# Performance work log

Measured on AMD Instinct MI355X. Metric: run time of the kernel, lower is better.

## Reference

```python
import jax, jax.numpy as jnp
import numpy as np

WS = 3  # window size


def _shift_stack(t_pad, D, H, W):
    # t_pad: [B, nh, hd, D+2p, H+2p, W+2p] -> [B, nh, hd, D, H, W, WS**3]
    slabs = [t_pad[..., i:i + D, j:j + H, l:l + W]
             for i in range(WS) for j in range(WS) for l in range(WS)]
    return jnp.stack(slabs, axis=-1)


def setup_inputs() -> dict:
    key = jax.random.key(0)
    ks = jax.random.split(key, 6)
    B, C, D, H, W = 2, 128, 24, 24, 24
    nh, hd = 4, 32
    return {
        "x": jax.random.normal(ks[0], (B, C, D, H, W), dtype=jnp.float32),
        "qkv_w": jax.random.normal(ks[1], (3 * C, C), dtype=jnp.float32) * 0.02,
        "qkv_b": jax.random.normal(ks[2], (3 * C,), dtype=jnp.float32) * 0.02,
        "proj_w": jax.random.normal(ks[3], (C, C), dtype=jnp.float32) * 0.02,
        "proj_b": jax.random.normal(ks[4], (C,), dtype=jnp.float32) * 0.02,
        "pos_embed": jax.random.normal(ks[5], (hd, WS, WS, WS), dtype=jnp.float32) * 0.02,
    }


def reference(x, qkv_w, qkv_b, proj_w, proj_b, pos_embed):
    B, C, D, H, W = x.shape
    hd = pos_embed.shape[0]
    nh = C // hd
    scale = hd ** -0.5
    pad = WS // 2

    # 1x1x1 Conv3d == pointwise linear over channel dim
    qkv = jnp.einsum('bcdhw,oc->bodhw', x, qkv_w) + qkv_b[None, :, None, None, None]
    q, k, v = jnp.split(qkv, 3, axis=1)
    q = q.reshape(B, nh, hd, D, H, W)
    k = k.reshape(B, nh, hd, D, H, W)
    v = v.reshape(B, nh, hd, D, H, W)

    pcfg = [(0, 0)] * 3 + [(pad, pad)] * 3
    k_pad = jnp.pad(k, pcfg)
    v_pad = jnp.pad(v, pcfg)

    # windows: [B, nh, hd, D, H, W, WS^3]; window center of q == q itself
    k_win = _shift_stack(k_pad, D, H, W)
    v_win = _shift_stack(v_pad, D, H, W)
    k_win = k_win + pos_embed.reshape(hd, WS ** 3)[None, None, :, None, None, None, :]

    scores = jnp.einsum('bncdhw,bncdhwk->bndhwk', q, k_win) * scale
    attn = jax.nn.softmax(scores, axis=-1)
    out = jnp.einsum('bndhwk,bncdhwk->bncdhw', attn, v_win)
    out = out.reshape(B, C, D, H, W)
    return jnp.einsum('bcdhw,oc->bodhw', out, proj_w) + proj_b[None, :, None, None, None]
```

## Files before the change

### kernel.cpp

```cpp
#include <hip/hip_runtime.h>
#include <hip/hip_bf16.h>
#include <hip/hip_fp16.h>

#define SVOX 13824
#define CIN 128
#define NHEAD 4
#define HDIM 32

#define BD 2
#define BH 4
#define BW 8
#define WD (BD+2)
#define WH (BH+2)
#define WW (BW+2)
#define NWIN (WD*WH*WW)

typedef __attribute__((ext_vector_type(8))) short short8;
typedef __attribute__((ext_vector_type(4))) float f32x4;
#if defined(__has_builtin)
#if __has_builtin(__builtin_amdgcn_fdot2_f32_bf16)
#define HAVE_DOT2BF 1
typedef __attribute__((ext_vector_type(2))) __bf16 bf16x2;
#endif
#if __has_builtin(__builtin_amdgcn_mov_dpp)
#define HAVE_DPP 1
#endif
#if __has_builtin(__builtin_amdgcn_cvt_pkrtz)
#define HAVE_PKRTZ 1
#endif
#endif

__device__ __forceinline__ unsigned short f2bf(float x) {
    unsigned u = __float_as_uint(x);
    u += 0x7FFFu + ((u >> 16) & 1u);
    return (unsigned short)(u >> 16);
}
__device__ __forceinline__ float dot2bf(unsigned a, unsigned b, float c) {
#ifdef HAVE_DOT2BF
    return __builtin_amdgcn_fdot2_f32_bf16(__builtin_bit_cast(bf16x2, a),
                                           __builtin_bit_cast(bf16x2, b), c, false);
#else
    return __uint_as_float(a << 16) * __uint_as_float(b << 16)
         + __uint_as_float(a & 0xffff0000u) * __uint_as_float(b & 0xffff0000u) + c;
#endif
}
template<int CTRL>
__device__ __forceinline__ float quad_dpp(float x) {
#ifdef HAVE_DPP
    return __int_as_float(__builtin_amdgcn_mov_dpp(__float_as_int(x), CTRL, 0xf, 0xf, true));
#else
    return __shfl_xor(x, (CTRL == 0xB1) ? 1 : 2);
#endif
}
__device__ __forceinline__ __half2 u2h2(unsigned u) {
    union { unsigned u; __half2 h; } c; c.u = u; return c.h;
}
__device__ __forceinline__ __half2 splat_h2(float x) {
#ifdef HAVE_PKRTZ
    auto v = __builtin_amdgcn_cvt_pkrtz(x, x);
    union { decltype(v) a; __half2 h; } c; c.a = v; return c.h;
#else
    return __float2half2_rn(x);
#endif
}
__device__ __forceinline__ unsigned short f2h(float x) {
    return __builtin_bit_cast(unsigned short, (_Float16)x);
}

__global__ __launch_bounds__(256) void qkv_gemm(
    const float* __restrict__ X,
    const float* __restrict__ W,
    const float* __restrict__ bias,
    const float* __restrict__ pos,
    unsigned* __restrict__ pe_out,
    ushort* __restrict__ q_out,
    ushort* __restrict__ k_out,
    ushort* __restrict__ v_out)
{
    __shared__ __align__(16) unsigned char smem[26624];
    ushort* Wb = (ushort*)smem;
    ushort* Xs = (ushort*)(smem + 17408);
    float*  T  = (float*)smem;

    const int t    = threadIdx.x;
    const int s0   = blockIdx.x * 64;
    const int o0   = blockIdx.y * 64;
    const int b    = blockIdx.z;
    const int lane = t & 63;
    const int wid  = t >> 6;
    const int l15  = lane & 15;
    const int g4   = lane >> 4;
    const int wm   = (wid >> 1) * 32;
    const int wn   = (wid & 1) * 32;

    if (blockIdx.x == 0 && blockIdx.y == 0 && blockIdx.z == 0 && t < 27 * 16) {
        int w = t >> 4, cp = t & 15;
        unsigned lo = f2bf(pos[(2 * cp) * 27 + w]);
        unsigned hi = f2bf(pos[(2 * cp + 1) * 27 + w]);
        pe_out[t] = lo | (hi << 16);
    }

    #pragma unroll
    for (int i = 0; i < 8; i++) {
        int f = t + i * 256;
        int row = f >> 5, c4 = f & 31;
        float4 w = *(const float4*)(W + (size_t)(o0 + row) * CIN + c4 * 4);
        ushort4 u;
        u.x = f2bf(w.x); u.y = f2bf(w.y); u.z = f2bf(w.z); u.w = f2bf(w.w);
        *(ushort4*)(Wb + row * 136 + c4 * 4) = u;
    }

    f32x4 acc[2][2];
    #pragma unroll
    for (int mf = 0; mf < 2; mf++)
        #pragma unroll
        for (int nf = 0; nf < 2; nf++)
            acc[mf][nf] = (f32x4){0.f, 0.f, 0.f, 0.f};

    const int sx = t & 63;
    const int kg = t >> 6;

    for (int chunk = 0; chunk < 2; chunk++) {
        __syncthreads();
        ushort xk[16];
        #pragma unroll
        for (int i = 0; i < 16; i++) {
            int k = kg * 16 + i;
            xk[i] = f2bf(X[((size_t)b * CIN + chunk * 64 + k) * SVOX + s0 + sx]);
        }
        #pragma unroll
        for (int j = 0; j < 2; j++) {
            short8 v;
            #pragma unroll
            for (int e = 0; e < 8; e++) v[e] = (short)xk[j * 8 + e];
            *(short8*)(Xs + sx * 72 + kg * 16 + j * 8) = v;
        }
        __syncthreads();

        #pragma unroll
        for (int ks = 0; ks < 2; ks++) {
            short8 Af[2], Bf[2];
            #pragma unroll
            for (int mf = 0; mf < 2; mf++)
                Af[mf] = *(const short8*)(Wb + (wm + mf * 16 + l15) * 136 + chunk * 64 + ks * 32 + g4 * 8);
            #pragma unroll
            for (int nf = 0; nf < 2; nf++)
                Bf[nf] = *(const short8*)(Xs + (wn + nf * 16 + l15) * 72 + ks * 32 + g4 * 8);
            #pragma unroll
            for (int mf = 0; mf < 2; mf++)
                #pragma unroll
                for (int nf = 0; nf < 2; nf++)
                    acc[mf][nf] = __builtin_amdgcn_mfma_f32_16x16x32_bf16(Af[mf], Bf[nf], acc[mf][nf], 0, 0, 0);
        }
    }

    __syncthreads();
    #pragma unroll
    for (int mf = 0; mf < 2; mf++)
        #pragma unroll
        for (int nf = 0; nf < 2; nf++) {
            int s  = wn + nf * 16 + l15;
            int mb = wm + mf * 16 + g4 * 4;
            *(f32x4*)(T + s * 68 + mb) = acc[mf][nf];
        }
    __syncthreads();
    #pragma unroll
    for (int i = 0; i < 4; i++) {
        int f = t + i * 256;
        int og = f & 15, sl = f >> 4;
        float4 v = *(float4*)(T + sl * 68 + og * 4);
        int o_g = o0 + og * 4;
        v.x += bias[o_g]; v.y += bias[o_g + 1]; v.z += bias[o_g + 2]; v.w += bias[o_g + 3];
        int part = o_g >> 7, pc = o_g & 127;
        int head = pc >> 5, ic = pc & 31;
        size_t base = (((size_t)b * NHEAD + head) * SVOX + s0 + sl) * HDIM + ic;
        ushort4 u;
        if (part == 2) {
            u.x = f2h(v.x); u.y = f2h(v.y); u.z = f2h(v.z); u.w = f2h(v.w);
        } else {
            u.x = f2bf(v.x); u.y = f2bf(v.y); u.z = f2bf(v.z); u.w = f2bf(v.w);
        }
        ushort* dst = (part == 0) ? q_out : (part == 1) ? k_out : v_out;
        *(ushort4*)(dst + base) = u;
    }
}

__global__ __launch_bounds__(256, 5) void attn_kernel(
    const ushort* __restrict__ qbf,
    const ushort* __restrict__ kbf,
    const ushort* __restrict__ vhf,
    const unsigned* __restrict__ pe_g,
    ushort* __restrict__ aout)
{
    __shared__ __align__(16) ushort Kl[NWIN * 32];
    __shared__ __align__(16) ushort Vl[NWIN * 32];

    const int t = threadIdx.x;
    const int br = blockIdx.x;
    const int n  = blockIdx.y;
    const int b  = blockIdx.z;
    const int bw_ = br % 3;
    const int bh_ = (br / 3) % 6;
    const int bd_ = br / 18;
    const int d0 = bd_ * BD, h0 = bh_ * BH, w0 = bw_ * BW;

    const ushort* kb = kbf + ((size_t)b * NHEAD + n) * (size_t)SVOX * HDIM;
    const ushort* vb = vhf + ((size_t)b * NHEAD + n) * (size_t)SVOX * HDIM;

    #pragma unroll
    for (int i = 0; i < 4; i++) {
        int f = t + i * 256;
        if (f < NWIN * 4) {
            int u = f >> 2, ch = f & 3;
            int ud = u / (WH * WW);
            int r  = u - ud * (WH * WW);
            int uh = r / WW;
            int uw = r - uh * WW;
            int gd = d0 + ud - 1, gh = h0 + uh - 1, gw = w0 + uw - 1;
            bool valid = ((unsigned)gd < 24u) & ((unsigned)gh < 24u) & ((unsigned)gw < 24u);
            size_t gsv = valid ? (size_t)(gd * 576 + gh * 24 + gw) : 0;
            uint4 kv = *(const uint4*)(kb + gsv * HDIM + ch * 8);
            uint4 vv = *(const uint4*)(vb + gsv * HDIM + ch * 8);
            if (!valid) { kv = make_uint4(0,0,0,0); vv = make_uint4(0,0,0,0); }
            *(uint4*)(Kl + u * 32 + ch * 8) = kv;
            *(uint4*)(Vl + u * 32 + ch * 8) = vv;
        }
    }

    const int p   = t >> 2;
    const int sub = t & 3;
    const int pw = p & 7, ph = (p >> 3) & 3, pd = p >> 5;
    const int sv = (d0 + pd) * 576 + (h0 + ph) * 24 + w0 + pw;
    uint4 qpk = *(const uint4*)(qbf + (((size_t)b * NHEAD + n) * SVOX + sv) * HDIM + sub * 8);

    float sc[27];
    #pragma unroll
    for (int s = 0; s < 27; s++) {
        uint4 pp = *(const uint4*)(pe_g + s * 16 + sub * 4);
        float a = dot2bf(qpk.x, pp.x, 0.f);
        a = dot2bf(qpk.y, pp.y, a);
        a = dot2bf(qpk.z, pp.z, a);
        a = dot2bf(qpk.w, pp.w, a);
        sc[s] = a;
    }

    __syncthreads();

    const int wc = (pd + 1) * (WH * WW) + (ph + 1) * WW + (pw + 1);
    const ushort* Kbase = Kl + wc * 32 + sub * 8;

    #pragma unroll
    for (int s = 0; s < 27; s++) {
        const int di = s / 9 - 1, dj = (s / 3) % 3 - 1, dl = s % 3 - 1;
        const int off = (di * (WH * WW) + dj * WW + dl) * 32;
        uint4 kk = *(const uint4*)(Kbase + off);
        float a = sc[s];
        a = dot2bf(qpk.x, kk.x, a);
        a = dot2bf(qpk.y, kk.y, a);
        a = dot2bf(qpk.z, kk.z, a);
        a = dot2bf(qpk.w, kk.w, a);
        sc[s] = a;
    }

    #pragma unroll
    for (int s = 0; s < 27; s++) {
        sc[s] += quad_dpp<0xB1>(sc[s]);
        sc[s] += quad_dpp<0x4E>(sc[s]);
    }

    float m3[9];
    #pragma unroll
    for (int j = 0; j < 9; j++)
        m3[j] = fmaxf(fmaxf(sc[3*j], sc[3*j+1]), sc[3*j+2]);
    float m9a = fmaxf(fmaxf(m3[0], m3[1]), m3[2]);
    float m9b = fmaxf(fmaxf(m3[3], m3[4]), m3[5]);
    float m9c = fmaxf(fmaxf(m3[6], m3[7]), m3[8]);
    float mx  = fmaxf(fmaxf(m9a, m9b), m9c);

    const float KS = 0.17677669529663687f * 1.4426950408889634f;
    float sum = 0.f;
    #pragma unroll
    for (int s = 0; s < 27; s++) {
        float e = exp2f((sc[s] - mx) * KS);
        sc[s] = e;
        sum += e;
    }
    float inv = 1.f / sum;

    const ushort* Vbase = Vl + wc * 32 + sub * 8;
    __half2 o2[4];
    __half2 hz = __float2half2_rn(0.f);
    o2[0] = hz; o2[1] = hz; o2[2] = hz; o2[3] = hz;
    #pragma unroll
    for (int s = 0; s < 27; s++) {
        const int di = s / 9 - 1, dj = (s / 3) % 3 - 1, dl = s % 3 - 1;
        const int off = (di * (WH * WW) + dj * WW + dl) * 32;
        uint4 vv = *(const uint4*)(Vbase + off);
        __half2 p2 = splat_h2(sc[s]);
        o2[0] = __hfma2(p2, u2h2(vv.x), o2[0]);
        o2[1] = __hfma2(p2, u2h2(vv.y), o2[1]);
        o2[2] = __hfma2(p2, u2h2(vv.z), o2[2]);
        o2[3] = __hfma2(p2, u2h2(vv.w), o2[3]);
    }

    float o[8];
    #pragma unroll
    for (int j = 0; j < 4; j++) {
        o[2*j]   = __low2float(o2[j]);
        o[2*j+1] = __high2float(o2[j]);
    }

    uint4 ou;
    ou.x = (unsigned)f2bf(o[0] * inv) | ((unsigned)f2bf(o[1] * inv) << 16);
    ou.y = (unsigned)f2bf(o[2] * inv) | ((unsigned)f2bf(o[3] * inv) << 16);
    ou.z = (unsigned)f2bf(o[4] * inv) | ((unsigned)f2bf(o[5] * inv) << 16);
    ou.w = (unsigned)f2bf(o[6] * inv) | ((unsigned)f2bf(o[7] * inv) << 16);
    *(uint4*)(aout + ((size_t)b * SVOX + sv) * CIN + n * HDIM + sub * 8) = ou;
}

__global__ __launch_bounds__(256) void proj_gemm(
    const ushort* __restrict__ Xa,
    const float* __restrict__ W,
    const float* __restrict__ bias,
    float* __restrict__ out)
{
    __shared__ __align__(16) unsigned char smem[34816];
    ushort* Wb = (ushort*)smem;
    ushort* Xs = (ushort*)(smem + 17408);
    float*  T  = (float*)smem;

    const int t    = threadIdx.x;
    const int s0   = blockIdx.x * 64;
    const int o0   = blockIdx.y * 64;
    const int b    = blockIdx.z;
    const int lane = t & 63;
    const int wid  = t >> 6;
    const int l15  = lane & 15;
    const int g4   = lane >> 4;
    const int wm   = (wid >> 1) * 32;
    const int wn   = (wid & 1) * 32;

    #pragma unroll
    for (int i = 0; i < 8; i++) {
        int f = t + i * 256;
        int row = f >> 5, c4 = f & 31;
        float4 w = *(const float4*)(W + (size_t)(o0 + row) * CIN + c4 * 4);
        ushort4 u;
        u.x = f2bf(w.x); u.y = f2bf(w.y); u.z = f2bf(w.z); u.w = f2bf(w.w);
        *(ushort4*)(Wb + row * 136 + c4 * 4) = u;
    }
    #pragma unroll
    for (int i = 0; i < 4; i++) {
        int f = t + i * 256;
        int row = f >> 4, c8 = f & 15;
        *(uint4*)(Xs + row * 136 + c8 * 8) =
            *(const uint4*)(Xa + ((size_t)b * SVOX + s0 + row) * CIN + c8 * 8);
    }
    __syncthreads();

    f32x4 acc[2][2];
    #pragma unroll
    for (int mf = 0; mf < 2; mf++)
        #pragma unroll
        for (int nf = 0; nf < 2; nf++)
            acc[mf][nf] = (f32x4){0.f, 0.f, 0.f, 0.f};

    #pragma unroll
    for (int ks = 0; ks < 4; ks++) {
        short8 Af[2], Bf[2];
        #pragma unroll
        for (int mf = 0; mf < 2; mf++)
            Af[mf] = *(const short8*)(Wb + (wm + mf * 16 + l15) * 136 + ks * 32 + g4 * 8);
        #pragma unroll
        for (int nf = 0; nf < 2; nf++)
            Bf[nf] = *(const short8*)(Xs + (wn + nf * 16 + l15) * 136 + ks * 32 + g4 * 8);
        #pragma unroll
        for (int mf = 0; mf < 2; mf++)
            #pragma unroll
            for (int nf = 0; nf < 2; nf++)
                acc[mf][nf] = __builtin_amdgcn_mfma_f32_16x16x32_bf16(Af[mf], Bf[nf], acc[mf][nf], 0, 0, 0);
    }

    __syncthreads();
    #pragma unroll
    for (int mf = 0; mf < 2; mf++)
        #pragma unroll
        for (int nf = 0; nf < 2; nf++) {
            int s  = wn + nf * 16 + l15;
            int mb = wm + mf * 16 + g4 * 4;
            #pragma unroll
            for (int r = 0; r < 4; r++)
                T[(mb + r) * 72 + s] = acc[mf][nf][r];
        }
    __syncthreads();
    #pragma unroll
    for (int i = 0; i < 4; i++) {
        int f = t + i * 256;
        int s4 = f & 15, m = f >> 4;
        float4 v = *(float4*)(T + m * 72 + s4 * 4);
        float bi = bias[o0 + m];
        v.x += bi; v.y += bi; v.z += bi; v.w += bi;
        *(float4*)(out + ((size_t)b * CIN + o0 + m) * SVOX + s0 + s4 * 4) = v;
    }
}

extern "C" void kernel_launch(void* const* d_in, const int* in_sizes, int n_in,
                              void* d_out, int out_size, void* d_ws, size_t ws_size,
                              hipStream_t stream) {
    const float* x      = (const float*)d_in[0];
    const float* qkv_w  = (const float*)d_in[1];
    const float* qkv_b  = (const float*)d_in[2];
    const float* proj_w = (const float*)d_in[3];
    const float* proj_b = (const float*)d_in[4];
    const float* pos    = (const float*)d_in[5];
    float* out = (float*)d_out;

    const size_t HSZ = (size_t)2 * NHEAD * SVOX * HDIM;
    ushort* qb  = (ushort*)d_ws;
    ushort* kbp = qb + HSZ;
    ushort* vbp = kbp + HSZ;
    ushort* attn_o = vbp + HSZ;
    unsigned* pe_p = (unsigned*)(attn_o + HSZ);

    qkv_gemm<<<dim3(SVOX/64, 384/64, 2), 256, 0, stream>>>(x, qkv_w, qkv_b, pos, pe_p, qb, kbp, vbp);
    attn_kernel<<<dim3(216, NHEAD, 2), 256, 0, stream>>>(qb, kbp, vbp, pe_p, attn_o);
    proj_gemm<<<dim3(SVOX/64, CIN/64, 2), 256, 0, stream>>>(attn_o, proj_w, proj_b, out);
}
```

Before: 46.32 us.

## Read V directly from global memory, drop LDS V tile and softmax max

Removes the shared-memory V staging and instead gathers the 27 neighbour V vectors straight from global memory, using a per-voxel validity mask so out-of-bounds neighbours get zero weight. This halves LDS use, so the launch-bounds occupancy hint is raised from 5 to 6 blocks. It also drops the max subtraction in softmax, which saves ALU work but risks exp overflow if scores get large, though that is unlikely at these input scales. Global V reads now depend on L2/L1 hits in place of LDS reuse.

```diff
diff --git a/kernel.cpp b/kernel.cpp
--- a/kernel.cpp
+++ b/kernel.cpp
@@ -185,7 +185,7 @@
     }
 }
 
-__global__ __launch_bounds__(256, 5) void attn_kernel(
+__global__ __launch_bounds__(256, 6) void attn_kernel(
     const ushort* __restrict__ qbf,
     const ushort* __restrict__ kbf,
     const ushort* __restrict__ vhf,
@@ -193,7 +193,6 @@
     ushort* __restrict__ aout)
 {
     __shared__ __align__(16) ushort Kl[NWIN * 32];
-    __shared__ __align__(16) ushort Vl[NWIN * 32];
 
     const int t = threadIdx.x;
     const int br = blockIdx.x;
@@ -220,18 +219,38 @@
             bool valid = ((unsigned)gd < 24u) & ((unsigned)gh < 24u) & ((unsigned)gw < 24u);
             size_t gsv = valid ? (size_t)(gd * 576 + gh * 24 + gw) : 0;
             uint4 kv = *(const uint4*)(kb + gsv * HDIM + ch * 8);
-            uint4 vv = *(const uint4*)(vb + gsv * HDIM + ch * 8);
-            if (!valid) { kv = make_uint4(0,0,0,0); vv = make_uint4(0,0,0,0); }
+            if (!valid) kv = make_uint4(0, 0, 0, 0);
             *(uint4*)(Kl + u * 32 + ch * 8) = kv;
-            *(uint4*)(Vl + u * 32 + ch * 8) = vv;
         }
     }
 
     const int p   = t >> 2;
     const int sub = t & 3;
     const int pw = p & 7, ph = (p >> 3) & 3, pd = p >> 5;
-    const int sv = (d0 + pd) * 576 + (h0 + ph) * 24 + w0 + pw;
+    const int dd0 = d0 + pd, hh0 = h0 + ph, ww0 = w0 + pw;
+    const int sv = dd0 * 576 + hh0 * 24 + ww0;
     uint4 qpk = *(const uint4*)(qbf + (((size_t)b * NHEAD + n) * SVOX + sv) * HDIM + sub * 8);
+
+    const int doff[27] = {
+        -601,-600,-599,-577,-576,-575,-553,-552,-551,
+         -25, -24, -23,  -1,   0,   1,  23,  24,  25,
+         551, 552, 553, 575, 576, 577, 599, 600, 601
+    };
+
+    unsigned vm = 0;
+    {
+        int widx = 0;
+        #pragma unroll
+        for (int di = -1; di <= 1; di++)
+        #pragma unroll
+        for (int dj = -1; dj <= 1; dj++)
+        #pragma unroll
+        for (int dl = -1; dl <= 1; dl++) {
+            if (((unsigned)(dd0 + di) < 24u) & ((unsigned)(hh0 + dj) < 24u) & ((unsigned)(ww0 + dl) < 24u))
+                vm |= 1u << widx;
+            widx++;
+        }
+    }
 
     float sc[27];
     #pragma unroll
@@ -268,35 +287,27 @@
         sc[s] += quad_dpp<0x4E>(sc[s]);
     }
 
-    float m3[9];
-    #pragma unroll
-    for (int j = 0; j < 9; j++)
-        m3[j] = fmaxf(fmaxf(sc[3*j], sc[3*j+1]), sc[3*j+2]);
-    float m9a = fmaxf(fmaxf(m3[0], m3[1]), m3[2]);
-    float m9b = fmaxf(fmaxf(m3[3], m3[4]), m3[5]);
-    float m9c = fmaxf(fmaxf(m3[6], m3[7]), m3[8]);
-    float mx  = fmaxf(fmaxf(m9a, m9b), m9c);
-
     const float KS = 0.17677669529663687f * 1.4426950408889634f;
     float sum = 0.f;
     #pragma unroll
     for (int s = 0; s < 27; s++) {
-        float e = exp2f((sc[s] - mx) * KS);
+        float e = exp2f(sc[s] * KS);
         sc[s] = e;
         sum += e;
     }
     float inv = 1.f / sum;
 
-    const ushort* Vbase = Vl + wc * 32 + sub * 8;
+    const ushort* Vbase = vb + (size_t)sv * HDIM + sub * 8;
     __half2 o2[4];
     __half2 hz = __float2half2_rn(0.f);
     o2[0] = hz; o2[1] = hz; o2[2] = hz; o2[3] = hz;
     #pragma unroll
     for (int s = 0; s < 27; s++) {
-        const int di = s / 9 - 1, dj = (s / 3) % 3 - 1, dl = s % 3 - 1;
-        const int off = (di * (WH * WW) + dj * WW + dl) * 32;
+        bool valid = (vm >> s) & 1u;
+        int off = valid ? doff[s] * 32 : 0;
         uint4 vv = *(const uint4*)(Vbase + off);
-        __half2 p2 = splat_h2(sc[s]);
+        float pr = valid ? sc[s] : 0.f;
+        __half2 p2 = splat_h2(pr);
         o2[0] = __hfma2(p2, u2h2(vv.x), o2[0]);
         o2[1] = __hfma2(p2, u2h2(vv.y), o2[1]);
         o2[2] = __hfma2(p2, u2h2(vv.z), o2[2]);
```

Measured after the change: 105.3 us. 127% more time.

## Split attention scores across quad lanes by window offset instead of channels

Applied to the files above, without the earlier changes.

Each of the four lanes per voxel now computes full 32-channel dot products for about 7 of the 27 window offsets, rather than a quarter of the channels for all 27. This removes the per-score cross-lane DPP reductions and cuts the per-thread score register footprint. Normalized probabilities are then shared to the quad with ds_bpermute during the V accumulation. The softmax max-subtraction is dropped, which relies on scores being small enough not to overflow exp. The attention output is now written as fp16 and the projection GEMM switches to f16 MFMA to match.

```diff
diff --git a/kernel.cpp b/kernel.cpp
--- a/kernel.cpp
+++ b/kernel.cpp
@@ -16,6 +16,7 @@
 #define NWIN (WD*WH*WW)
 
 typedef __attribute__((ext_vector_type(8))) short short8;
+typedef __attribute__((ext_vector_type(8))) _Float16 half8;
 typedef __attribute__((ext_vector_type(4))) float f32x4;
 #if defined(__has_builtin)
 #if __has_builtin(__builtin_amdgcn_fdot2_f32_bf16)
@@ -55,12 +56,13 @@
 __device__ __forceinline__ __half2 u2h2(unsigned u) {
     union { unsigned u; __half2 h; } c; c.u = u; return c.h;
 }
-__device__ __forceinline__ __half2 splat_h2(float x) {
+__device__ __forceinline__ unsigned splat_h2u(float x) {
 #ifdef HAVE_PKRTZ
     auto v = __builtin_amdgcn_cvt_pkrtz(x, x);
-    union { decltype(v) a; __half2 h; } c; c.a = v; return c.h;
+    union { decltype(v) a; unsigned u; } c; c.a = v; return c.u;
 #else
-    return __float2half2_rn(x);
+    __half2 h = __float2half2_rn(x);
+    union { __half2 h; unsigned u; } c; c.h = h; return c.u;
 #endif
 }
 __device__ __forceinline__ unsigned short f2h(float x) {
@@ -194,6 +196,7 @@
 {
     __shared__ __align__(16) ushort Kl[NWIN * 32];
     __shared__ __align__(16) ushort Vl[NWIN * 32];
+    __shared__ int doffT[32];
 
     const int t = threadIdx.x;
     const int br = blockIdx.x;
@@ -203,6 +206,11 @@
     const int bh_ = (br / 3) % 6;
     const int bd_ = br / 18;
     const int d0 = bd_ * BD, h0 = bh_ * BH, w0 = bw_ * BW;
+
+    if (t < 27) {
+        int di = t / 9 - 1, dj = (t / 3) % 3 - 1, dl = t % 3 - 1;
+        doffT[t] = (di * (WH * WW) + dj * WW + dl) * 64;
+    }
 
     const ushort* kb = kbf + ((size_t)b * NHEAD + n) * (size_t)SVOX * HDIM;
     const ushort* vb = vhf + ((size_t)b * NHEAD + n) * (size_t)SVOX * HDIM;
@@ -231,61 +239,68 @@
     const int sub = t & 3;
     const int pw = p & 7, ph = (p >> 3) & 3, pd = p >> 5;
     const int sv = (d0 + pd) * 576 + (h0 + ph) * 24 + w0 + pw;
-    uint4 qpk = *(const uint4*)(qbf + (((size_t)b * NHEAD + n) * SVOX + sv) * HDIM + sub * 8);
-
-    float sc[27];
-    #pragma unroll
-    for (int s = 0; s < 27; s++) {
-        uint4 pp = *(const uint4*)(pe_g + s * 16 + sub * 4);
-        float a = dot2bf(qpk.x, pp.x, 0.f);
-        a = dot2bf(qpk.y, pp.y, a);
-        a = dot2bf(qpk.z, pp.z, a);
-        a = dot2bf(qpk.w, pp.w, a);
-        sc[s] = a;
+
+    const ushort* qrow = qbf + (((size_t)b * NHEAD + n) * SVOX + sv) * HDIM;
+    uint4 q0 = *(const uint4*)(qrow);
+    uint4 q1 = *(const uint4*)(qrow + 8);
+    uint4 q2 = *(const uint4*)(qrow + 16);
+    uint4 q3 = *(const uint4*)(qrow + 24);
+
+    float sc[7];
+    #pragma unroll
+    for (int i = 0; i < 7; i++) {
+        int s = 4 * i + sub; s = (s > 26) ? 26 : s;
+        const uint4* pp = (const uint4*)(pe_g + s * 16);
+        uint4 p0 = pp[0], p1 = pp[1], p2 = pp[2], p3 = pp[3];
+        float a = dot2bf(q0.x, p0.x, 0.f);
+        a = dot2bf(q0.y, p0.y, a); a = dot2bf(q0.z, p0.z, a); a = dot2bf(q0.w, p0.w, a);
+        a = dot2bf(q1.x, p1.x, a); a = dot2bf(q1.y, p1.y, a); a = dot2bf(q1.z, p1.z, a); a = dot2bf(q1.w, p1.w, a);
+        a = dot2bf(q2.x, p2.x, a); a = dot2bf(q2.y, p2.y, a); a = dot2bf(q2.z, p2.z, a); a = dot2bf(q2.w, p2.w, a);
+        a = dot2bf(q3.x, p3.x, a); a = dot2bf(q3.y, p3.y, a); a = dot2bf(q3.z, p3.z, a); a = dot2bf(q3.w, p3.w, a);
+        sc[i] = a;
     }
 
     __syncthreads();
 
     const int wc = (pd + 1) * (WH * WW) + (ph + 1) * WW + (pw + 1);
-    const ushort* Kbase = Kl + wc * 32 + sub * 8;
-
-    #pragma unroll
-    for (int s = 0; s < 27; s++) {
-        const int di = s / 9 - 1, dj = (s / 3) % 3 - 1, dl = s % 3 - 1;
-        const int off = (di * (WH * WW) + dj * WW + dl) * 32;
-        uint4 kk = *(const uint4*)(Kbase + off);
-        float a = sc[s];
-        a = dot2bf(qpk.x, kk.x, a);
-        a = dot2bf(qpk.y, kk.y, a);
-        a = dot2bf(qpk.z, kk.z, a);
-        a = dot2bf(qpk.w, kk.w, a);
-        sc[s] = a;
-    }
-
-    #pragma unroll
-    for (int s = 0; s < 27; s++) {
-        sc[s] += quad_dpp<0xB1>(sc[s]);
-        sc[s] += quad_dpp<0x4E>(sc[s]);
-    }
-
-    float m3[9];
-    #pragma unroll
-    for (int j = 0; j < 9; j++)
-        m3[j] = fmaxf(fmaxf(sc[3*j], sc[3*j+1]), sc[3*j+2]);
-    float m9a = fmaxf(fmaxf(m3[0], m3[1]), m3[2]);
-    float m9b = fmaxf(fmaxf(m3[3], m3[4]), m3[5]);
-    float m9c = fmaxf(fmaxf(m3[6], m3[7]), m3[8]);
-    float mx  = fmaxf(fmaxf(m9a, m9b), m9c);
+    const char* KrowB = (const char*)Kl + wc * 64;
+
+    #pragma unroll
+    for (int i = 0; i < 7; i++) {
+        int s = 4 * i + sub; s = (s > 26) ? 26 : s;
+        const ushort* kp = (const ushort*)(KrowB + doffT[s]);
+        uint4 k0 = *(const uint4*)(kp);
+        uint4 k1 = *(const uint4*)(kp + 8);
+        uint4 k2 = *(const uint4*)(kp + 16);
+        uint4 k3 = *(const uint4*)(kp + 24);
+        float a = sc[i];
+        a = dot2bf(q0.x, k0.x, a); a = dot2bf(q0.y, k0.y, a); a = dot2bf(q0.z, k0.z, a); a = dot2bf(q0.w, k0.w, a);
+        a = dot2bf(q1.x, k1.x, a); a = dot2bf(q1.y, k1.y, a); a = dot2bf(q1.z, k1.z, a); a = dot2bf(q1.w, k1.w, a);
+        a = dot2bf(q2.x, k2.x, a); a = dot2bf(q2.y, k2.y, a); a = dot2bf(q2.z, k2.z, a); a = dot2bf(q2.w, k2.w, a);
+        a = dot2bf(q3.x, k3.x, a); a = dot2bf(q3.y, k3.y, a); a = dot2bf(q3.z, k3.z, a); a = dot2bf(q3.w, k3.w, a);
+        sc[i] = a;
+    }
 
     const float KS = 0.17677669529663687f * 1.4426950408889634f;
-    float sum = 0.f;
-    #pragma unroll
-    for (int s = 0; s < 27; s++) {
-        float e = exp2f((sc[s] - mx) * KS);
-        sc[s] = e;
-        sum += e;
-    }
-    float inv = 1.f / sum;
+    float e[7];
+    float sm = 0.f;
+    #pragma unroll
+    for (int i = 0; i < 7; i++) {
+        float ee = exp2f(sc[i] * KS);
+        if (4 * i + sub > 26) ee = 0.f;
+        e[i] = ee;
+        sm += ee;
+    }
+    sm += quad_dpp<0xB1>(sm);
+    sm += quad_dpp<0x4E>(sm);
+    float inv = 1.f / sm;
+
+    unsigned ph2[7];
+    #pragma unroll
+    for (int i = 0; i < 7; i++)
+        ph2[i] = splat_h2u(e[i] * inv);
+
+    const int lb = ((t & 63) & ~3) * 4;
 
     const ushort* Vbase = Vl + wc * 32 + sub * 8;
     __half2 o2[4];
@@ -295,27 +310,18 @@
     for (int s = 0; s < 27; s++) {
         const int di = s / 9 - 1, dj = (s / 3) % 3 - 1, dl = s % 3 - 1;
         const int off = (di * (WH * WW) + dj * WW + dl) * 32;
+        int src = __builtin_amdgcn_ds_bpermute(lb + (s & 3) * 4, (int)ph2[s >> 2]);
+        __half2 p2 = u2h2((unsigned)src);
         uint4 vv = *(const uint4*)(Vbase + off);
-        __half2 p2 = splat_h2(sc[s]);
         o2[0] = __hfma2(p2, u2h2(vv.x), o2[0]);
         o2[1] = __hfma2(p2, u2h2(vv.y), o2[1]);
         o2[2] = __hfma2(p2, u2h2(vv.z), o2[2]);
         o2[3] = __hfma2(p2, u2h2(vv.w), o2[3]);
     }
 
-    float o[8];
-    #pragma unroll
-    for (int j = 0; j < 4; j++) {
-        o[2*j]   = __low2float(o2[j]);
-        o[2*j+1] = __high2float(o2[j]);
-    }
-
-    uint4 ou;
-    ou.x = (unsigned)f2bf(o[0] * inv) | ((unsigned)f2bf(o[1] * inv) << 16);
-    ou.y = (unsigned)f2bf(o[2] * inv) | ((unsigned)f2bf(o[3] * inv) << 16);
-    ou.z = (unsigned)f2bf(o[4] * inv) | ((unsigned)f2bf(o[5] * inv) << 16);
-    ou.w = (unsigned)f2bf(o[6] * inv) | ((unsigned)f2bf(o[7] * inv) << 16);
-    *(uint4*)(aout + ((size_t)b * SVOX + sv) * CIN + n * HDIM + sub * 8) = ou;
+    union { __half2 h[4]; uint4 u; } ou;
+    ou.h[0] = o2[0]; ou.h[1] = o2[1]; ou.h[2] = o2[2]; ou.h[3] = o2[3];
+    *(uint4*)(aout + ((size_t)b * SVOX + sv) * CIN + n * HDIM + sub * 8) = ou.u;
 }
 
 __global__ __launch_bounds__(256) void proj_gemm(
@@ -346,7 +352,7 @@
         int row = f >> 5, c4 = f & 31;
         float4 w = *(const float4*)(W + (size_t)(o0 + row) * CIN + c4 * 4);
         ushort4 u;
-        u.x = f2bf(w.x); u.y = f2bf(w.y); u.z = f2bf(w.z); u.w = f2bf(w.w);
+        u.x = f2h(w.x); u.y = f2h(w.y); u.z = f2h(w.z); u.w = f2h(w.w);
         *(ushort4*)(Wb + row * 136 + c4 * 4) = u;
     }
     #pragma unroll
@@ -367,18 +373,18 @@
 
     #pragma unroll
     for (int ks = 0; ks < 4; ks++) {
-        short8 Af[2], Bf[2];
+        half8 Af[2], Bf[2];
         #pragma unroll
         for (int mf = 0; mf < 2; mf++)
-            Af[mf] = *(const short8*)(Wb + (wm + mf * 16 + l15) * 136 + ks * 32 + g4 * 8);
+            Af[mf] = __builtin_bit_cast(half8, *(const short8*)(Wb + (wm + mf * 16 + l15) * 136 + ks * 32 + g4 * 8));
         #pragma unroll
         for (int nf = 0; nf < 2; nf++)
-            Bf[nf] = *(const short8*)(Xs + (wn + nf * 16 + l15) * 136 + ks * 32 + g4 * 8);
+            Bf[nf] = __builtin_bit_cast(half8, *(const short8*)(Xs + (wn + nf * 16 + l15) * 136 + ks * 32 + g4 * 8));
         #pragma unroll
         for (int mf = 0; mf < 2; mf++)
             #pragma unroll
             for (int nf = 0; nf < 2; nf++)
-                acc[mf][nf] = __builtin_amdgcn_mfma_f32_16x16x32_bf16(Af[mf], Bf[nf], acc[mf][nf], 0, 0, 0);
+                acc[mf][nf] = __builtin_amdgcn_mfma_f32_16x16x32_f16(Af[mf], Bf[nf], acc[mf][nf], 0, 0, 0);
     }
 
     __syncthreads();
```

Result: slower. 48.45 us (+4.6%).

## Process two adjacent query voxels per thread to share K/V window loads

Applied to the files above, without the earlier changes.

Each thread now handles an even/odd pair of neighbouring voxels along W. The pair shares the overlapping K and V LDS reads, 36 loads instead of 54. The tile doubles in H (BH 8) to keep 256 threads, the halo ratio drops, and the grid halves. Softmax drops the max subtraction and the output is written as fp16, with proj_gemm switched to fp16 MFMA to match. Risks are overflow in exp without max subtraction, higher register pressure (launch bounds 5 to 3) and fp16 precision changes.

```diff
diff --git a/kernel.cpp b/kernel.cpp
--- a/kernel.cpp
+++ b/kernel.cpp
@@ -8,7 +8,7 @@
 #define HDIM 32
 
 #define BD 2
-#define BH 4
+#define BH 8
 #define BW 8
 #define WD (BD+2)
 #define WH (BH+2)
@@ -16,6 +16,7 @@
 #define NWIN (WD*WH*WW)
 
 typedef __attribute__((ext_vector_type(8))) short short8;
+typedef __attribute__((ext_vector_type(8))) _Float16 half8;
 typedef __attribute__((ext_vector_type(4))) float f32x4;
 #if defined(__has_builtin)
 #if __has_builtin(__builtin_amdgcn_fdot2_f32_bf16)
@@ -43,6 +44,11 @@
     return __uint_as_float(a << 16) * __uint_as_float(b << 16)
          + __uint_as_float(a & 0xffff0000u) * __uint_as_float(b & 0xffff0000u) + c;
 #endif
+}
+__device__ __forceinline__ float dot4(uint4 a, uint4 b, float c) {
+    c = dot2bf(a.x, b.x, c); c = dot2bf(a.y, b.y, c);
+    c = dot2bf(a.z, b.z, c); c = dot2bf(a.w, b.w, c);
+    return c;
 }
 template<int CTRL>
 __device__ __forceinline__ float quad_dpp(float x) {
@@ -185,7 +191,7 @@
     }
 }
 
-__global__ __launch_bounds__(256, 5) void attn_kernel(
+__global__ __launch_bounds__(256, 3) void attn_kernel(
     const ushort* __restrict__ qbf,
     const ushort* __restrict__ kbf,
     const ushort* __restrict__ vhf,
@@ -200,15 +206,15 @@
     const int n  = blockIdx.y;
     const int b  = blockIdx.z;
     const int bw_ = br % 3;
-    const int bh_ = (br / 3) % 6;
-    const int bd_ = br / 18;
+    const int bh_ = (br / 3) % 3;
+    const int bd_ = br / 9;
     const int d0 = bd_ * BD, h0 = bh_ * BH, w0 = bw_ * BW;
 
     const ushort* kb = kbf + ((size_t)b * NHEAD + n) * (size_t)SVOX * HDIM;
     const ushort* vb = vhf + ((size_t)b * NHEAD + n) * (size_t)SVOX * HDIM;
 
     #pragma unroll
-    for (int i = 0; i < 4; i++) {
+    for (int i = 0; i < 7; i++) {
         int f = t + i * 256;
         if (f < NWIN * 4) {
             int u = f >> 2, ch = f & 3;
@@ -227,95 +233,101 @@
         }
     }
 
-    const int p   = t >> 2;
+    const int qd  = t >> 2;
     const int sub = t & 3;
-    const int pw = p & 7, ph = (p >> 3) & 3, pd = p >> 5;
-    const int sv = (d0 + pd) * 576 + (h0 + ph) * 24 + w0 + pw;
-    uint4 qpk = *(const uint4*)(qbf + (((size_t)b * NHEAD + n) * SVOX + sv) * HDIM + sub * 8);
-
-    float sc[27];
+    const int pw2 = qd & 3;
+    const int ph  = (qd >> 2) & 7;
+    const int pd  = qd >> 5;
+    const int pwE = pw2 * 2;
+    const int svE = (d0 + pd) * 576 + (h0 + ph) * 24 + w0 + pwE;
+
+    const ushort* qrow = qbf + (((size_t)b * NHEAD + n) * SVOX + svE) * HDIM + sub * 8;
+    uint4 qE = *(const uint4*)(qrow);
+    uint4 qO = *(const uint4*)(qrow + HDIM);
+
+    float scE[27], scO[27];
     #pragma unroll
     for (int s = 0; s < 27; s++) {
         uint4 pp = *(const uint4*)(pe_g + s * 16 + sub * 4);
-        float a = dot2bf(qpk.x, pp.x, 0.f);
-        a = dot2bf(qpk.y, pp.y, a);
-        a = dot2bf(qpk.z, pp.z, a);
-        a = dot2bf(qpk.w, pp.w, a);
-        sc[s] = a;
-    }
-
-    __syncthreads();
-
-    const int wc = (pd + 1) * (WH * WW) + (ph + 1) * WW + (pw + 1);
-    const ushort* Kbase = Kl + wc * 32 + sub * 8;
+        scE[s] = dot4(qE, pp, 0.f);
+        scO[s] = dot4(qO, pp, 0.f);
+    }
+
+    __syncthreads();
+
+    const int wcE = (pd + 1) * (WH * WW) + (ph + 1) * WW + (pwE + 1);
+    const ushort* Kbase = Kl + wcE * 32 + sub * 8;
+
+    #pragma unroll
+    for (int di = 0; di < 3; di++)
+    #pragma unroll
+    for (int dj = 0; dj < 3; dj++)
+    #pragma unroll
+    for (int dlp = 0; dlp < 4; dlp++) {
+        const int off = ((di - 1) * (WH * WW) + (dj - 1) * WW + (dlp - 1)) * 32;
+        uint4 kk = *(const uint4*)(Kbase + off);
+        if (dlp <= 2) { const int s = (di * 3 + dj) * 3 + dlp;     scE[s] = dot4(qE, kk, scE[s]); }
+        if (dlp >= 1) { const int s = (di * 3 + dj) * 3 + dlp - 1; scO[s] = dot4(qO, kk, scO[s]); }
+    }
 
     #pragma unroll
     for (int s = 0; s < 27; s++) {
-        const int di = s / 9 - 1, dj = (s / 3) % 3 - 1, dl = s % 3 - 1;
-        const int off = (di * (WH * WW) + dj * WW + dl) * 32;
-        uint4 kk = *(const uint4*)(Kbase + off);
-        float a = sc[s];
-        a = dot2bf(qpk.x, kk.x, a);
-        a = dot2bf(qpk.y, kk.y, a);
-        a = dot2bf(qpk.z, kk.z, a);
-        a = dot2bf(qpk.w, kk.w, a);
-        sc[s] = a;
-    }
-
+        scE[s] += quad_dpp<0xB1>(scE[s]);
+        scE[s] += quad_dpp<0x4E>(scE[s]);
+        scO[s] += quad_dpp<0xB1>(scO[s]);
+        scO[s] += quad_dpp<0x4E>(scO[s]);
+    }
+
+    const float KS = 0.17677669529663687f * 1.4426950408889634f;
+    float sumE = 0.f, sumO = 0.f;
     #pragma unroll
     for (int s = 0; s < 27; s++) {
-        sc[s] += quad_dpp<0xB1>(sc[s]);
-        sc[s] += quad_dpp<0x4E>(sc[s]);
-    }
-
-    float m3[9];
-    #pragma unroll
-    for (int j = 0; j < 9; j++)
-        m3[j] = fmaxf(fmaxf(sc[3*j], sc[3*j+1]), sc[3*j+2]);
-    float m9a = fmaxf(fmaxf(m3[0], m3[1]), m3[2]);
-    float m9b = fmaxf(fmaxf(m3[3], m3[4]), m3[5]);
-    float m9c = fmaxf(fmaxf(m3[6], m3[7]), m3[8]);
-    float mx  = fmaxf(fmaxf(m9a, m9b), m9c);
-
-    const float KS = 0.17677669529663687f * 1.4426950408889634f;
-    float sum = 0.f;
-    #pragma unroll
-    for (int s = 0; s < 27; s++) {
-        float e = exp2f((sc[s] - mx) * KS);
-        sc[s] = e;
-        sum += e;
-    }
-    float inv = 1.f / sum;
-
-    const ushort* Vbase = Vl + wc * 32 + sub * 8;
-    __half2 o2[4];
+        float eE = exp2f(scE[s] * KS);
+        float eO = exp2f(scO[s] * KS);
+        scE[s] = eE; sumE += eE;
+        scO[s] = eO; sumO += eO;
+    }
+    float invE = 1.f / sumE, invO = 1.f / sumO;
+    #pragma unroll
+    for (int s = 0; s < 27; s++) { scE[s] *= invE; scO[s] *= invO; }
+
+    const ushort* Vbase = Vl + wcE * 32 + sub * 8;
+    __half2 oE[4], oO[4];
     __half2 hz = __float2half2_rn(0.f);
-    o2[0] = hz; o2[1] = hz; o2[2] = hz; o2[3] = hz;
-    #pragma unroll
-    for (int s = 0; s < 27; s++) {
-        const int di = s / 9 - 1, dj = (s / 3) % 3 - 1, dl = s % 3 - 1;
-        const int off = (di * (WH * WW) + dj * WW + dl) * 32;
+    oE[0]=hz; oE[1]=hz; oE[2]=hz; oE[3]=hz;
+    oO[0]=hz; oO[1]=hz; oO[2]=hz; oO[3]=hz;
+    #pragma unroll
+    for (int di = 0; di < 3; di++)
+    #pragma unroll
+    for (int dj = 0; dj < 3; dj++)
+    #pragma unroll
+    for (int dlp = 0; dlp < 4; dlp++) {
+        const int off = ((di - 1) * (WH * WW) + (dj - 1) * WW + (dlp - 1)) * 32;
         uint4 vv = *(const uint4*)(Vbase + off);
-        __half2 p2 = splat_h2(sc[s]);
-        o2[0] = __hfma2(p2, u2h2(vv.x), o2[0]);
-        o2[1] = __hfma2(p2, u2h2(vv.y), o2[1]);
-        o2[2] = __hfma2(p2, u2h2(vv.z), o2[2]);
-        o2[3] = __hfma2(p2, u2h2(vv.w), o2[3]);
-    }
-
-    float o[8];
-    #pragma unroll
-    for (int j = 0; j < 4; j++) {
-        o[2*j]   = __low2float(o2[j]);
-        o[2*j+1] = __high2float(o2[j]);
-    }
-
-    uint4 ou;
-    ou.x = (unsigned)f2bf(o[0] * inv) | ((unsigned)f2bf(o[1] * inv) << 16);
-    ou.y = (unsigned)f2bf(o[2] * inv) | ((unsigned)f2bf(o[3] * inv) << 16);
-    ou.z = (unsigned)f2bf(o[4] * inv) | ((unsigned)f2bf(o[5] * inv) << 16);
-    ou.w = (unsigned)f2bf(o[6] * inv) | ((unsigned)f2bf(o[7] * inv) << 16);
-    *(uint4*)(aout + ((size_t)b * SVOX + sv) * CIN + n * HDIM + sub * 8) = ou;
+        if (dlp <= 2) {
+            const int s = (di * 3 + dj) * 3 + dlp;
+            __half2 p2 = splat_h2(scE[s]);
+            oE[0] = __hfma2(p2, u2h2(vv.x), oE[0]);
+            oE[1] = __hfma2(p2, u2h2(vv.y), oE[1]);
+            oE[2] = __hfma2(p2, u2h2(vv.z), oE[2]);
+            oE[3] = __hfma2(p2, u2h2(vv.w), oE[3]);
+        }
+        if (dlp >= 1) {
+            const int s = (di * 3 + dj) * 3 + dlp - 1;
+            __half2 p2 = splat_h2(scO[s]);
+            oO[0] = __hfma2(p2, u2h2(vv.x), oO[0]);
+            oO[1] = __hfma2(p2, u2h2(vv.y), oO[1]);
+            oO[2] = __hfma2(p2, u2h2(vv.z), oO[2]);
+            oO[3] = __hfma2(p2, u2h2(vv.w), oO[3]);
+        }
+    }
+
+    union { __half2 h[4]; uint4 u; } ouE, ouO;
+    ouE.h[0]=oE[0]; ouE.h[1]=oE[1]; ouE.h[2]=oE[2]; ouE.h[3]=oE[3];
+    ouO.h[0]=oO[0]; ouO.h[1]=oO[1]; ouO.h[2]=oO[2]; ouO.h[3]=oO[3];
+    ushort* op = aout + ((size_t)b * SVOX + svE) * CIN + n * HDIM + sub * 8;
+    *(uint4*)(op)       = ouE.u;
+    *(uint4*)(op + CIN) = ouO.u;
 }
 
 __global__ __launch_bounds__(256) void proj_gemm(
@@ -346,7 +358,7 @@
         int row = f >> 5, c4 = f & 31;
         float4 w = *(const float4*)(W + (size_t)(o0 + row) * CIN + c4 * 4);
         ushort4 u;
-        u.x = f2bf(w.x); u.y = f2bf(w.y); u.z = f2bf(w.z); u.w = f2bf(w.w);
+        u.x = f2h(w.x); u.y = f2h(w.y); u.z = f2h(w.z); u.w = f2h(w.w);
         *(ushort4*)(Wb + row * 136 + c4 * 4) = u;
     }
     #pragma unroll
@@ -367,18 +379,18 @@
 
     #pragma unroll
     for (int ks = 0; ks < 4; ks++) {
-        short8 Af[2], Bf[2];
+        half8 Af[2], Bf[2];
         #pragma unroll
         for (int mf = 0; mf < 2; mf++)
-            Af[mf] = *(const short8*)(Wb + (wm + mf * 16 + l15) * 136 + ks * 32 + g4 * 8);
+            Af[mf] = __builtin_bit_cast(half8, *(const short8*)(Wb + (wm + mf * 16 + l15) * 136 + ks * 32 + g4 * 8));
         #pragma unroll
         for (int nf = 0; nf < 2; nf++)
-            Bf[nf] = *(const short8*)(Xs + (wn + nf * 16 + l15) * 136 + ks * 32 + g4 * 8);
+            Bf[nf] = __builtin_bit_cast(half8, *(const short8*)(Xs + (wn + nf * 16 + l15) * 136 + ks * 32 + g4 * 8));
         #pragma unroll
         for (int mf = 0; mf < 2; mf++)
             #pragma unroll
             for (int nf = 0; nf < 2; nf++)
-                acc[mf][nf] = __builtin_amdgcn_mfma_f32_16x16x32_bf16(Af[mf], Bf[nf], acc[mf][nf], 0, 0, 0);
+                acc[mf][nf] = __builtin_amdgcn_mfma_f32_16x16x32_f16(Af[mf], Bf[nf], acc[mf][nf], 0, 0, 0);
     }
 
     __syncthreads();
@@ -423,6 +435,6 @@
     unsigned* pe_p = (unsigned*)(attn_o + HSZ);
 
     qkv_gemm<<<dim3(SVOX/64, 384/64, 2), 256, 0, stream>>>(x, qkv_w, qkv_b, pos, pe_p, qb, kbp, vbp);
-    attn_kernel<<<dim3(216, NHEAD, 2), 256, 0, stream>>>(qb, kbp, vbp, pe_p, attn_o);
+    attn_kernel<<<dim3(108, NHEAD, 2), 256, 0, stream>>>(qb, kbp, vbp, pe_p, attn_o);
     proj_gemm<<<dim3(SVOX/64, CIN/64, 2), 256, 0, stream>>>(attn_o, proj_w, proj_b, out);
 }
```

Result: slower. 47.28 us (+2.1%).
